# Kernel tuning notes

Hardware: AMD Instinct MI355X
Metric: run time of the kernel (lower is better)

Reference implementation:

```python
import jax, jax.numpy as jnp
import numpy as np

NUM_EXPERTS = 16
IN_FEATURES = 2048
OUT_FEATURES = 2048
RANK = 128
ALPHA = 32.0
TOKENS = 32768  # total packed tokens, multiple of NUM_EXPERTS (pad_seq_to_mult guarantees this)


def setup_inputs() -> dict:
    key = jax.random.key(0)
    k1, k2, k3 = jax.random.split(key, 3)
    x = jax.random.normal(k1, (TOKENS, IN_FEATURES), dtype=jnp.float32)
    # linear_in per-expert weights (kaiming-style random for reference)
    lora_a = jax.random.normal(k2, (NUM_EXPERTS, IN_FEATURES, RANK), dtype=jnp.float32) * (1.0 / np.sqrt(IN_FEATURES))
    # linear_out per-expert weights (LoRA convention init is zeros; random here for nontrivial check)
    lora_b = jax.random.normal(k3, (NUM_EXPERTS, RANK, OUT_FEATURES), dtype=jnp.float32) * (1.0 / np.sqrt(RANK))
    return {"x": x, "lora_a": lora_a, "lora_b": lora_b}


def reference(x, lora_a, lora_b):
    # Tokens are packed per expert with uniform counts (padding to a multiple of
    # NUM_EXPERTS is handled upstream by pad_seq_to_mult). Grouped LoRA:
    #   out_e = (x_e @ A_e) @ B_e * (alpha / rank)
    E = lora_a.shape[0]
    T, H = x.shape
    xg = x.reshape(E, T // E, H)                      # [E, Te, H]
    low = jnp.einsum('eth,ehr->etr', xg, lora_a)      # grouped GEMM 1: [E, Te, r]
    # activation = identity (adapter default)
    out = jnp.einsum('etr,ero->eto', low, lora_b)     # grouped GEMM 2: [E, Te, O]
    scale = ALPHA / RANK
    return (out * scale).reshape(T, -1)               # [T, O]
```

## Files before the change

### kernel.cpp

```cpp
#include <hip/hip_runtime.h>
#include <hip/hip_bf16.h>
#include <stdint.h>

#define NEXP   16
#define TTOK   32768
#define HIN    2048
#define RNK    128
#define OOUT   2048
#define TE     (TTOK / NEXP)
#define LORA_SCALE 0.25f

typedef __bf16 bf16_t;
typedef bf16_t bf16x8 __attribute__((ext_vector_type(8)));
typedef float  f32x4  __attribute__((ext_vector_type(4)));

__global__ void transpose_cvt_kernel(const float* __restrict__ src,
                                     bf16_t* __restrict__ dst,
                                     int Rr, int Cc)
{
    __shared__ float tile[32][33];
    const int e  = blockIdx.z;
    const int c0 = blockIdx.x * 32;
    const int r0 = blockIdx.y * 32;
    const float* s = src + (size_t)e * Rr * Cc;
    bf16_t*      d = dst + (size_t)e * Rr * Cc;
    const int tx = threadIdx.x & 31;
    const int ty = threadIdx.x >> 5;
#pragma unroll
    for (int j = 0; j < 32; j += 8)
        tile[ty + j][tx] = s[(size_t)(r0 + ty + j) * Cc + (c0 + tx)];
    __syncthreads();
#pragma unroll
    for (int j = 0; j < 32; j += 8)
        d[(size_t)(c0 + ty + j) * Rr + (r0 + tx)] = (bf16_t)tile[tx][ty + j];
}

__global__ __launch_bounds__(256)
void gemm_grouped_bt(const float* __restrict__ A,
                     const bf16_t* __restrict__ Bt,
                     float* __restrict__ C,
                     int K, int N, float scale)
{
    const int tid  = threadIdx.x;
    const int brow = blockIdx.x;
    const int bcol = blockIdx.y;
    const int expert = brow / (TE / 128);
    const int row0 = brow * 128;
    const int col0 = bcol * 128;

    __shared__ bf16_t As[128 * 32];
    __shared__ bf16_t Bs[128 * 32];

    const int wave = tid >> 6;
    const int lane = tid & 63;
    const int wr = (wave >> 1) * 64;
    const int wc = (wave & 1) * 64;
    const int lm = lane & 15;
    const int q  = lane >> 4;

    f32x4 acc[4][4] = {};

    const float*  Ag = A  + (size_t)row0 * K;
    const bf16_t* Bg = Bt + ((size_t)expert * N + col0) * K;

    const int sidx0 = tid * 8;
    const int sr0 = sidx0 >> 5, sk0 = sidx0 & 31;
    const int sidx1 = 2048 + tid * 8;
    const int sr1 = sidx1 >> 5, sk1 = sidx1 & 31;

    for (int k0 = 0; k0 < K; k0 += 32) {
        const float* pa0 = Ag + (size_t)sr0 * K + k0 + sk0;
        const float* pa1 = Ag + (size_t)sr1 * K + k0 + sk1;
        f32x4 a0lo = *(const f32x4*)pa0;
        f32x4 a0hi = *(const f32x4*)(pa0 + 4);
        f32x4 a1lo = *(const f32x4*)pa1;
        f32x4 a1hi = *(const f32x4*)(pa1 + 4);
        bf16x8 b0 = *(const bf16x8*)(Bg + (size_t)sr0 * K + k0 + sk0);
        bf16x8 b1 = *(const bf16x8*)(Bg + (size_t)sr1 * K + k0 + sk1);

        bf16x8 a0, a1;
#pragma unroll
        for (int i = 0; i < 4; ++i) {
            a0[i]     = (bf16_t)a0lo[i];
            a0[4 + i] = (bf16_t)a0hi[i];
            a1[i]     = (bf16_t)a1lo[i];
            a1[4 + i] = (bf16_t)a1hi[i];
        }

        *(bf16x8*)(As + sidx0) = a0;
        *(bf16x8*)(As + sidx1) = a1;
        *(bf16x8*)(Bs + sidx0) = b0;
        *(bf16x8*)(Bs + sidx1) = b1;
        __syncthreads();

        bf16x8 af[4], bfr[4];
#pragma unroll
        for (int rt = 0; rt < 4; ++rt)
            af[rt] = *(const bf16x8*)(As + (wr + rt * 16 + lm) * 32 + q * 8);
#pragma unroll
        for (int ct = 0; ct < 4; ++ct)
            bfr[ct] = *(const bf16x8*)(Bs + (wc + ct * 16 + lm) * 32 + q * 8);

#pragma unroll
        for (int rt = 0; rt < 4; ++rt)
#pragma unroll
            for (int ct = 0; ct < 4; ++ct)
                acc[rt][ct] = __builtin_amdgcn_mfma_f32_16x16x32_bf16(
                    af[rt], bfr[ct], acc[rt][ct], 0, 0, 0);

        __syncthreads();
    }

#pragma unroll
    for (int rt = 0; rt < 4; ++rt) {
#pragma unroll
        for (int i = 0; i < 4; ++i) {
            const int grow = row0 + wr + rt * 16 + q * 4 + i;
            float* Crow = C + (size_t)grow * N + col0 + wc;
#pragma unroll
            for (int ct = 0; ct < 4; ++ct)
                Crow[ct * 16 + lm] = acc[rt][ct][i] * scale;
        }
    }
}

extern "C" void kernel_launch(void* const* d_in, const int* in_sizes, int n_in,
                              void* d_out, int out_size, void* d_ws, size_t ws_size,
                              hipStream_t stream)
{
    const float* x  = (const float*)d_in[0];
    const float* la = (const float*)d_in[1];
    const float* lb = (const float*)d_in[2];
    float* out = (float*)d_out;

    bf16_t* At  = (bf16_t*)d_ws;
    bf16_t* Btw = At + (size_t)NEXP * RNK * HIN;
    float*  low = (float*)(Btw + (size_t)NEXP * OOUT * RNK);

    {
        dim3 g(RNK / 32, HIN / 32, NEXP);
        transpose_cvt_kernel<<<g, 256, 0, stream>>>(la, At, HIN, RNK);
    }
    {
        dim3 g(OOUT / 32, RNK / 32, NEXP);
        transpose_cvt_kernel<<<g, 256, 0, stream>>>(lb, Btw, RNK, OOUT);
    }
    {
        dim3 g(TTOK / 128, RNK / 128);
        gemm_grouped_bt<<<g, 256, 0, stream>>>(x, At, low, HIN, RNK, 1.0f);
    }
    {
        dim3 g(TTOK / 128, OOUT / 128);
        gemm_grouped_bt<<<g, 256, 0, stream>>>(low, Btw, out, RNK, OOUT, LORA_SCALE);
    }
}
```

Before: 544.5 us.

## Fuse both grouped LoRA GEMMs into one kernel keeping low-rank tile in LDS

Replaces the two separate grouped GEMM launches with one fused kernel. Each 512-thread block computes a 128x128 low-rank tile of x@A, keeps it in LDS as bf16, then sweeps all output columns against B. This removes the fp32 intermediate round trip through global memory and a kernel launch. It also adds double-buffered LDS with register prefetch and XOR-swizzled LDS layouts. The trade-off is 96KB of LDS per block and only 256 blocks, which may limit occupancy, and the intermediate is now rounded to bf16 before the second GEMM.

Result: faster. 526.7 us (-3.3%).

```diff
diff --git a/kernel.cpp b/kernel.cpp
--- a/kernel.cpp
+++ b/kernel.cpp
@@ -12,6 +12,7 @@
 
 typedef __bf16 bf16_t;
 typedef bf16_t bf16x8 __attribute__((ext_vector_type(8)));
+typedef bf16_t bf16x4 __attribute__((ext_vector_type(4)));
 typedef float  f32x4  __attribute__((ext_vector_type(4)));
 
 __global__ void transpose_cvt_kernel(const float* __restrict__ src,
@@ -35,92 +36,188 @@
         d[(size_t)(c0 + ty + j) * Rr + (r0 + tx)] = (bf16_t)tile[tx][ty + j];
 }
 
-__global__ __launch_bounds__(256)
-void gemm_grouped_bt(const float* __restrict__ A,
-                     const bf16_t* __restrict__ Bt,
-                     float* __restrict__ C,
-                     int K, int N, float scale)
+__global__ __launch_bounds__(512, 2)
+void fused_lora(const float* __restrict__ X,
+                const bf16_t* __restrict__ Atw,
+                const bf16_t* __restrict__ Btw,
+                float* __restrict__ Out)
 {
+    __shared__ __align__(16) char lds[98304];
+
     const int tid  = threadIdx.x;
-    const int brow = blockIdx.x;
-    const int bcol = blockIdx.y;
-    const int expert = brow / (TE / 128);
-    const int row0 = brow * 128;
-    const int col0 = bcol * 128;
-
-    __shared__ bf16_t As[128 * 32];
-    __shared__ bf16_t Bs[128 * 32];
+    const int blk  = blockIdx.x;
+    const int m0   = blk * 128;
+    const int e    = blk >> 4;
 
     const int wave = tid >> 6;
     const int lane = tid & 63;
-    const int wr = (wave >> 1) * 64;
-    const int wc = (wave & 1) * 64;
-    const int lm = lane & 15;
-    const int q  = lane >> 4;
-
-    f32x4 acc[4][4] = {};
-
-    const float*  Ag = A  + (size_t)row0 * K;
-    const bf16_t* Bg = Bt + ((size_t)expert * N + col0) * K;
-
-    const int sidx0 = tid * 8;
-    const int sr0 = sidx0 >> 5, sk0 = sidx0 & 31;
-    const int sidx1 = 2048 + tid * 8;
-    const int sr1 = sidx1 >> 5, sk1 = sidx1 & 31;
-
-    for (int k0 = 0; k0 < K; k0 += 32) {
-        const float* pa0 = Ag + (size_t)sr0 * K + k0 + sk0;
-        const float* pa1 = Ag + (size_t)sr1 * K + k0 + sk1;
-        f32x4 a0lo = *(const f32x4*)pa0;
-        f32x4 a0hi = *(const f32x4*)(pa0 + 4);
-        f32x4 a1lo = *(const f32x4*)pa1;
-        f32x4 a1hi = *(const f32x4*)(pa1 + 4);
-        bf16x8 b0 = *(const bf16x8*)(Bg + (size_t)sr0 * K + k0 + sk0);
-        bf16x8 b1 = *(const bf16x8*)(Bg + (size_t)sr1 * K + k0 + sk1);
-
-        bf16x8 a0, a1;
+    const int lm   = lane & 15;
+    const int q    = lane >> 4;
+    const int wr   = (wave >> 1) * 32;
+    const int wc   = (wave & 1) * 64;
+
+    const int sr  = tid >> 2;
+    const int sc  = tid & 3;
+    const int ssw = (sr & 7) << 4;
+
+    const float*  xg = X   + (size_t)(m0 + sr) * HIN + sc * 16;
+    const bf16_t* ag = Atw + ((size_t)e * RNK + sr) * HIN + sc * 16;
+
+    f32x4  xa[4];
+    bf16x8 ar[2];
+    f32x4  acc1[2][4] = {};
+
+    {
+#pragma unroll
+        for (int i = 0; i < 4; ++i) xa[i] = *(const f32x4*)(xg + i * 4);
+        ar[0] = *(const bf16x8*)(ag);
+        ar[1] = *(const bf16x8*)(ag + 8);
+        bf16x8 c0, c1;
 #pragma unroll
         for (int i = 0; i < 4; ++i) {
-            a0[i]     = (bf16_t)a0lo[i];
-            a0[4 + i] = (bf16_t)a0hi[i];
-            a1[i]     = (bf16_t)a1lo[i];
-            a1[4 + i] = (bf16_t)a1hi[i];
-        }
-
-        *(bf16x8*)(As + sidx0) = a0;
-        *(bf16x8*)(As + sidx1) = a1;
-        *(bf16x8*)(Bs + sidx0) = b0;
-        *(bf16x8*)(Bs + sidx1) = b1;
+            c0[i] = (bf16_t)xa[0][i]; c0[4 + i] = (bf16_t)xa[1][i];
+            c1[i] = (bf16_t)xa[2][i]; c1[4 + i] = (bf16_t)xa[3][i];
+        }
+        char* bx = lds + sr * 128;
+        *(bf16x8*)(bx + ((sc * 32     ) ^ ssw)) = c0;
+        *(bf16x8*)(bx + ((sc * 32 + 16) ^ ssw)) = c1;
+        char* ba = lds + 32768 + sr * 128;
+        *(bf16x8*)(ba + ((sc * 32     ) ^ ssw)) = ar[0];
+        *(bf16x8*)(ba + ((sc * 32 + 16) ^ ssw)) = ar[1];
+    }
+    __syncthreads();
+
+    for (int it = 0; it < 32; ++it) {
+        const int cur = it & 1;
+        if (it < 31) {
+            const float*  px = xg + (it + 1) * 64;
+            const bf16_t* pa = ag + (it + 1) * 64;
+#pragma unroll
+            for (int i = 0; i < 4; ++i) xa[i] = *(const f32x4*)(px + i * 4);
+            ar[0] = *(const bf16x8*)(pa);
+            ar[1] = *(const bf16x8*)(pa + 8);
+        }
+        const char* xb = lds + cur * 16384;
+        const char* ab = lds + 32768 + cur * 16384;
+#pragma unroll
+        for (int ks = 0; ks < 2; ++ks) {
+            bf16x8 XF[2], AF[4];
+#pragma unroll
+            for (int mt = 0; mt < 2; ++mt) {
+                const int row = wr + mt * 16 + lm;
+                XF[mt] = *(const bf16x8*)(xb + row * 128 +
+                           ((ks * 64 + q * 16) ^ ((row & 7) << 4)));
+            }
+#pragma unroll
+            for (int rt = 0; rt < 4; ++rt) {
+                const int row = wc + rt * 16 + lm;
+                AF[rt] = *(const bf16x8*)(ab + row * 128 +
+                           ((ks * 64 + q * 16) ^ ((row & 7) << 4)));
+            }
+#pragma unroll
+            for (int mt = 0; mt < 2; ++mt)
+#pragma unroll
+                for (int rt = 0; rt < 4; ++rt)
+                    acc1[mt][rt] = __builtin_amdgcn_mfma_f32_16x16x32_bf16(
+                        AF[rt], XF[mt], acc1[mt][rt], 0, 0, 0);
+        }
+        if (it < 31) {
+            bf16x8 c0, c1;
+#pragma unroll
+            for (int i = 0; i < 4; ++i) {
+                c0[i] = (bf16_t)xa[0][i]; c0[4 + i] = (bf16_t)xa[1][i];
+                c1[i] = (bf16_t)xa[2][i]; c1[4 + i] = (bf16_t)xa[3][i];
+            }
+            char* bx = lds + (cur ^ 1) * 16384 + sr * 128;
+            *(bf16x8*)(bx + ((sc * 32     ) ^ ssw)) = c0;
+            *(bf16x8*)(bx + ((sc * 32 + 16) ^ ssw)) = c1;
+            char* ba = lds + 32768 + (cur ^ 1) * 16384 + sr * 128;
+            *(bf16x8*)(ba + ((sc * 32     ) ^ ssw)) = ar[0];
+            *(bf16x8*)(ba + ((sc * 32 + 16) ^ ssw)) = ar[1];
+        }
         __syncthreads();
-
-        bf16x8 af[4], bfr[4];
-#pragma unroll
-        for (int rt = 0; rt < 4; ++rt)
-            af[rt] = *(const bf16x8*)(As + (wr + rt * 16 + lm) * 32 + q * 8);
-#pragma unroll
-        for (int ct = 0; ct < 4; ++ct)
-            bfr[ct] = *(const bf16x8*)(Bs + (wc + ct * 16 + lm) * 32 + q * 8);
-
-#pragma unroll
-        for (int rt = 0; rt < 4; ++rt)
-#pragma unroll
-            for (int ct = 0; ct < 4; ++ct)
-                acc[rt][ct] = __builtin_amdgcn_mfma_f32_16x16x32_bf16(
-                    af[rt], bfr[ct], acc[rt][ct], 0, 0, 0);
-
+    }
+
+    bf16x8 br[4];
+    const bf16_t* bg0 = Btw + ((size_t)e * OOUT + sr) * RNK + sc * 32;
+#pragma unroll
+    for (int i = 0; i < 4; ++i) br[i] = *(const bf16x8*)(bg0 + i * 8);
+
+    char* Lbase = lds + 65536;
+#pragma unroll
+    for (int mt = 0; mt < 2; ++mt) {
+        const int m   = wr + mt * 16 + lm;
+        const int msw = (m & 7) << 4;
+#pragma unroll
+        for (int rt = 0; rt < 4; ++rt) {
+            const int r0 = wc + rt * 16 + q * 4;
+            bf16x4 v;
+#pragma unroll
+            for (int i = 0; i < 4; ++i) v[i] = (bf16_t)acc1[mt][rt][i];
+            *(bf16x4*)(Lbase + m * 256 + ((r0 * 2) ^ msw)) = v;
+        }
+    }
+    __syncthreads();
+
+    bf16x8 af2[2][4];
+#pragma unroll
+    for (int mt = 0; mt < 2; ++mt) {
+        const int m   = wr + mt * 16 + lm;
+        const int msw = (m & 7) << 4;
+#pragma unroll
+        for (int ks = 0; ks < 4; ++ks)
+            af2[mt][ks] = *(const bf16x8*)(Lbase + m * 256 +
+                             ((ks * 64 + q * 16) ^ msw));
+    }
+
+    {
+        char* bb = lds + sr * 256;
+#pragma unroll
+        for (int i = 0; i < 4; ++i)
+            *(bf16x8*)(bb + ((sc * 64 + i * 16) ^ ssw)) = br[i];
+    }
+    __syncthreads();
+
+    for (int c = 0; c < 16; ++c) {
+        const int cur = c & 1;
+        if (c < 15) {
+            const bf16_t* bg = bg0 + (size_t)(c + 1) * 128 * RNK;
+#pragma unroll
+            for (int i = 0; i < 4; ++i) br[i] = *(const bf16x8*)(bg + i * 8);
+        }
+        f32x4 acc2[2][4] = {};
+        const char* bb = lds + cur * 32768;
+#pragma unroll
+        for (int nt = 0; nt < 4; ++nt) {
+            const int n   = wc + nt * 16 + lm;
+            const int nsw = (n & 7) << 4;
+#pragma unroll
+            for (int ks = 0; ks < 4; ++ks) {
+                const bf16x8 bfr = *(const bf16x8*)(bb + n * 256 +
+                                      ((ks * 64 + q * 16) ^ nsw));
+                acc2[0][nt] = __builtin_amdgcn_mfma_f32_16x16x32_bf16(
+                    bfr, af2[0][ks], acc2[0][nt], 0, 0, 0);
+                acc2[1][nt] = __builtin_amdgcn_mfma_f32_16x16x32_bf16(
+                    bfr, af2[1][ks], acc2[1][nt], 0, 0, 0);
+            }
+        }
+#pragma unroll
+        for (int mt = 0; mt < 2; ++mt) {
+            const int gm = m0 + wr + mt * 16 + lm;
+            float* orow = Out + (size_t)gm * OOUT + c * 128 + wc + q * 4;
+#pragma unroll
+            for (int nt = 0; nt < 4; ++nt) {
+                const f32x4 v = acc2[mt][nt] * LORA_SCALE;
+                *(f32x4*)(orow + nt * 16) = v;
+            }
+        }
+        if (c < 15) {
+            char* bb2 = lds + (cur ^ 1) * 32768 + sr * 256;
+#pragma unroll
+            for (int i = 0; i < 4; ++i)
+                *(bf16x8*)(bb2 + ((sc * 64 + i * 16) ^ ssw)) = br[i];
+        }
         __syncthreads();
-    }
-
-#pragma unroll
-    for (int rt = 0; rt < 4; ++rt) {
-#pragma unroll
-        for (int i = 0; i < 4; ++i) {
-            const int grow = row0 + wr + rt * 16 + q * 4 + i;
-            float* Crow = C + (size_t)grow * N + col0 + wc;
-#pragma unroll
-            for (int ct = 0; ct < 4; ++ct)
-                Crow[ct * 16 + lm] = acc[rt][ct][i] * scale;
-        }
     }
 }
 
@@ -135,7 +232,6 @@
 
     bf16_t* At  = (bf16_t*)d_ws;
     bf16_t* Btw = At + (size_t)NEXP * RNK * HIN;
-    float*  low = (float*)(Btw + (size_t)NEXP * OOUT * RNK);
 
     {
         dim3 g(RNK / 32, HIN / 32, NEXP);
@@ -145,12 +241,5 @@
         dim3 g(OOUT / 32, RNK / 32, NEXP);
         transpose_cvt_kernel<<<g, 256, 0, stream>>>(lb, Btw, RNK, OOUT);
     }
-    {
-        dim3 g(TTOK / 128, RNK / 128);
-        gemm_grouped_bt<<<g, 256, 0, stream>>>(x, At, low, HIN, RNK, 1.0f);
-    }
-    {
-        dim3 g(TTOK / 128, OOUT / 128);
-        gemm_grouped_bt<<<g, 256, 0, stream>>>(low, Btw, out, RNK, OOUT, LORA_SCALE);
-    }
+    fused_lora<<<dim3(TTOK / 128), dim3(512), 0, stream>>>(x, At, Btw, out);
 }
```
